# Kernel optimization log

Measured on AMD Instinct MI355X. Metric: run time of the kernel, lower is better.

The kernel has to match this reference:

```python
import jax, jax.numpy as jnp
import numpy as np

B, N_VIS, N_TOT, D, H, DEPTH = 4, 512, 2048, 768, 8, 2
HID = 3072  # int(D * 4.0)
TOKEN_DIM = 768


def setup_inputs() -> dict:
    key = jax.random.key(0)
    ks = jax.random.split(key, 20)
    s = 0.02
    # mask: exactly N_VIS True per row (visible positions), random placement
    u = jax.random.uniform(ks[0], (B, N_TOT))
    rank = jnp.argsort(jnp.argsort(u, axis=1), axis=1)
    mask = rank < N_VIS
    inp = {
        'visible_tokens': jax.random.normal(ks[1], (B, N_VIS, D), jnp.float32),
        'mask': mask,
        'mask_token': jax.random.normal(ks[2], (D,), jnp.float32) * s,
        'gamma1': jnp.ones((DEPTH, D), jnp.float32),
        'beta1': jnp.zeros((DEPTH, D), jnp.float32),
        'Wqkv': jax.random.normal(ks[3], (DEPTH, 3 * D, D), jnp.float32) * s,
        'bqkv': jnp.zeros((DEPTH, 3 * D), jnp.float32),
        'Wo': jax.random.normal(ks[4], (DEPTH, D, D), jnp.float32) * s,
        'bo': jnp.zeros((DEPTH, D), jnp.float32),
        'gamma2': jnp.ones((DEPTH, D), jnp.float32),
        'beta2': jnp.zeros((DEPTH, D), jnp.float32),
        'W1': jax.random.normal(ks[5], (DEPTH, HID, D), jnp.float32) * s,
        'b1': jnp.zeros((DEPTH, HID), jnp.float32),
        'W2': jax.random.normal(ks[6], (DEPTH, D, HID), jnp.float32) * s,
        'b2': jnp.zeros((DEPTH, D), jnp.float32),
        'gn': jnp.ones((D,), jnp.float32),
        'gb': jnp.zeros((D,), jnp.float32),
        'Wdec': jax.random.normal(ks[7], (TOKEN_DIM, D), jnp.float32) * s,
        'bdec': jnp.zeros((TOKEN_DIM,), jnp.float32),
    }
    return inp


def layer_norm(x, g, b, eps=1e-5):
    mu = jnp.mean(x, axis=-1, keepdims=True)
    var = jnp.var(x, axis=-1, keepdims=True)
    return (x - mu) * jax.lax.rsqrt(var + eps) * g + b


def mha(x, Wqkv, bqkv, Wo, bo):
    Bq, N, Dm = x.shape
    dh = Dm // H
    qkv = x @ Wqkv.T + bqkv  # (B,N,3D)
    q, k, v = jnp.split(qkv, 3, axis=-1)
    q = q.reshape(Bq, N, H, dh).transpose(0, 2, 1, 3)
    k = k.reshape(Bq, N, H, dh).transpose(0, 2, 1, 3)
    v = v.reshape(Bq, N, H, dh).transpose(0, 2, 1, 3)
    scores = jnp.einsum('bhqd,bhkd->bhqk', q, k) / jnp.sqrt(jnp.float32(dh))
    attn = jax.nn.softmax(scores, axis=-1)
    out = jnp.einsum('bhqk,bhkd->bhqd', attn, v)
    out = out.transpose(0, 2, 1, 3).reshape(Bq, N, Dm)
    return out @ Wo.T + bo


def decoder_block(x, g1, be1, Wqkv, bqkv, Wo, bo, g2, be2, W1f, b1f, W2f, b2f):
    x = x + mha(layer_norm(x, g1, be1), Wqkv, bqkv, Wo, bo)
    h = layer_norm(x, g2, be2)
    h = jax.nn.gelu(h @ W1f.T + b1f, approximate=False)
    return x + h @ W2f.T + b2f


def reference(visible_tokens, mask, mask_token, gamma1, beta1, Wqkv, bqkv, Wo, bo,
              gamma2, beta2, W1, b1, W2, b2, gn, gb, Wdec, bdec):
    # Vectorized in-order scatter: position n gets visible token #(count of True in mask[:, :n+1]) - 1
    idx = jnp.clip(jnp.cumsum(mask.astype(jnp.int32), axis=1) - 1, 0, N_VIS - 1)  # (B, N_TOT)
    gathered = jnp.take_along_axis(visible_tokens, idx[..., None], axis=1)  # (B, N_TOT, D)
    x = jnp.where(mask[..., None], gathered, mask_token)
    for i in range(DEPTH):
        x = decoder_block(x, gamma1[i], beta1[i], Wqkv[i], bqkv[i], Wo[i], bo[i],
                          gamma2[i], beta2[i], W1[i], b1[i], W2[i], b2[i])
    x = layer_norm(x, gn, gb)
    return x @ Wdec.T + bdec  # (B, N_TOT, token_dim)
```

## Files before the change

### kernel.cpp

```cpp
#include <hip/hip_runtime.h>
#include <stdint.h>

typedef __attribute__((ext_vector_type(8))) __bf16 bf16x8;
typedef __attribute__((ext_vector_type(4))) float f32x4;

#define DEVI static __device__ __forceinline__

#define QK_SCALE 0.10206207261596577f

DEVI uint16_t f2bf(float f){
  union{float f; uint32_t u;} v; v.f=f;
  uint32_t u = v.u;
  uint32_t r = u + 0x7FFFu + ((u>>16)&1u);
  return (uint16_t)(r>>16);
}
DEVI void gload16(const void* g, void* l){
  __builtin_amdgcn_global_load_lds((const __attribute__((address_space(1))) unsigned int*)g,
                                   (__attribute__((address_space(3))) unsigned int*)l, 16, 0, 0);
}


__global__ void cvt4_f32_bf16(const float* __restrict__ a, int na, uint16_t* __restrict__ oa,
                              const float* __restrict__ b, int nb, uint16_t* __restrict__ ob,
                              const float* __restrict__ c, int nc, uint16_t* __restrict__ oc,
                              const float* __restrict__ d, int nd, uint16_t* __restrict__ od){
  int total = na+nb+nc+nd;
  int stride = gridDim.x*blockDim.x;
  for(int i = blockIdx.x*blockDim.x + threadIdx.x; i<total; i+=stride){
    int j = i;
    if(j < na){ oa[j] = f2bf(a[j]); continue; }
    j -= na;
    if(j < nb){ ob[j] = f2bf(b[j]); continue; }
    j -= nb;
    if(j < nc){ oc[j] = f2bf(c[j]); continue; }
    j -= nc;
    od[j] = f2bf(d[j]);
  }
}

__global__ void cvt_wqkv(const float* __restrict__ in, uint16_t* __restrict__ out){
  const int n = 2*2304*768;
  int i = blockIdx.x*blockDim.x + threadIdx.x;
  int stride = gridDim.x*blockDim.x;
  for(; i<n; i+=stride){
    float v = in[i];
    if(((i/768) % 2304) < 768) v *= QK_SCALE;
    out[i] = f2bf(v);
  }
}

__global__ void scale_bqkv(const float* __restrict__ in, float* __restrict__ out){
  int i = blockIdx.x*blockDim.x + threadIdx.x;
  if(i < 2*2304){
    float v = in[i];
    if((i % 2304) < 768) v *= QK_SCALE;
    out[i] = v;
  }
}

__global__ void detect_mask(const uint8_t* __restrict__ mask, int* __restrict__ flag){
  __shared__ int cnt;
  if(threadIdx.x==0) cnt=0;
  __syncthreads();
  int c=0;
  for(int i=threadIdx.x;i<2048;i+=blockDim.x) c += (mask[i]!=0) ? 1 : 0;
  atomicAdd(&cnt, c);
  __syncthreads();
  if(threadIdx.x==0) *flag = (cnt==512) ? 1 : 0;
}

__global__ void scatter_idx(const void* __restrict__ maskp, const int* __restrict__ flag,
                            int* __restrict__ idx, uint8_t* __restrict__ mb){
  int b = blockIdx.x;
  int t = threadIdx.x;
  int f = *flag;
  const uint8_t* m8  = (const uint8_t*)maskp + (size_t)b*2048;
  const int*     m32 = (const int*)maskp + (size_t)b*2048;
  int v[8]; int s=0;
  for(int j=0;j<8;j++){ int n=t*8+j; int mv = f ? (m8[n]!=0) : (m32[n]!=0); v[j]=mv; s+=mv; }
  __shared__ int ps[256];
  ps[t]=s; __syncthreads();
  int acc=0;
  for(int i=0;i<t;i++) acc += ps[i];
  int cum=acc;
  for(int j=0;j<8;j++){
    int n=t*8+j;
    cum += v[j];
    int id = cum-1; id = id<0?0:(id>511?511:id);
    idx[(size_t)b*2048+n]=id;
    mb[(size_t)b*2048+n]=(uint8_t)v[j];
  }
}

__global__ void build_x(const float* __restrict__ vis, const float* __restrict__ mtok,
                        const int* __restrict__ idx, const uint8_t* __restrict__ mb,
                        float* __restrict__ x){
  int bn = blockIdx.x;
  int b = bn>>11;
  int id = idx[bn]; int m = mb[bn];
  const float* src = m ? (vis + ((size_t)b*512 + id)*768) : mtok;
  float* dst = x + (size_t)bn*768;
  for(int d=threadIdx.x; d<768; d+=256) dst[d] = src[d];
}

__global__ __launch_bounds__(256) void ln_kernel(const float* __restrict__ x,
                const float* __restrict__ g, const float* __restrict__ be,
                uint16_t* __restrict__ out){
  int row = blockIdx.x; int t = threadIdx.x;
  const float* xr = x + (size_t)row*768;
  float a0=xr[t], a1=xr[t+256], a2=xr[t+512];
  float s=a0+a1+a2, q=a0*a0+a1*a1+a2*a2;
  for(int off=32; off>0; off>>=1){ s+=__shfl_xor(s,off,64); q+=__shfl_xor(q,off,64); }
  __shared__ float sh[8];
  int w=t>>6, l=t&63;
  if(l==0){ sh[w]=s; sh[4+w]=q; }
  __syncthreads();
  s = sh[0]+sh[1]+sh[2]+sh[3];
  q = sh[4]+sh[5]+sh[6]+sh[7];
  float mean = s*(1.f/768.f);
  float var  = q*(1.f/768.f) - mean*mean;
  float rstd = rsqrtf(var + 1e-5f);
  uint16_t* orow = out + (size_t)row*768;
  orow[t]     = f2bf((a0-mean)*rstd*g[t]     + be[t]);
  orow[t+256] = f2bf((a1-mean)*rstd*g[t+256] + be[t+256]);
  orow[t+512] = f2bf((a2-mean)*rstd*g[t+512] + be[t+512]);
}

__global__ __launch_bounds__(128) void vtrans_kernel(const uint16_t* __restrict__ qkv,
                                                     uint16_t* __restrict__ vt){
  int nc = blockIdx.x, bh = blockIdx.y;
  int b = bh >> 3, h = bh & 7;
  int d = threadIdx.x;
  if(d >= 96) return;
  const uint16_t* src = qkv + ((size_t)(b*2048 + nc*8))*2304 + 1536 + h*96 + d;
  uint16_t vbuf[8];
  #pragma unroll
  for(int j=0;j<8;j++) vbuf[j] = src[(size_t)j*2304];
  *(uint4*)&vt[((size_t)bh*96 + d)*2048 + nc*8] = *(const uint4*)vbuf;
}

template<int BM, int BN, int WGM, int WGN, int GELU, int OUTF32>
__global__ __launch_bounds__(WGM*WGN*64) void gemm_kernel(const uint16_t* __restrict__ A,
        const uint16_t* __restrict__ W, const float* __restrict__ bias,
        const float* __restrict__ resid, void* __restrict__ outp,
        int M, int N, int K){
  constexpr int THREADS = WGM*WGN*64;
  constexpr int WTM = BM/WGM, WTN = BN/WGN;
  constexpr int MFM = WTM/16, MFN = WTN/16;
  constexpr int NCA = BM*4/THREADS;
  constexpr int NCB = BN*4/THREADS;
  __shared__ uint16_t sA[2][BM*32];
  __shared__ uint16_t sB[2][BN*32];
  int tid = threadIdx.x;
  int l = tid & 63, w = tid >> 6;
  int row0 = blockIdx.x*BM, col0 = blockIdx.y*BN;
  int wm = w / WGN, wn = w % WGN;
  f32x4 zero = {0.f,0.f,0.f,0.f};
  f32x4 acc[MFM][MFN];
  #pragma unroll
  for(int m=0;m<MFM;m++)
    #pragma unroll
    for(int n=0;n<MFN;n++) acc[m][n]=zero;
  int lr = l&15, lk = (l>>4)*8;
  int nkt = K >> 5;

  const uint16_t* gaP[NCA]; int ldsA[NCA];
  const uint16_t* gbP[NCB]; int ldsB[NCB];
  #pragma unroll
  for(int c=0;c<NCA;c++){
    int cb = c*THREADS + w*64;
    int ch = cb + l;
    gaP[c] = A + (size_t)(row0 + (ch>>2))*K + (ch&3)*8;
    ldsA[c] = cb*16;
  }
  #pragma unroll
  for(int c=0;c<NCB;c++){
    int cb = c*THREADS + w*64;
    int ch = cb + l;
    gbP[c] = W + (size_t)(col0 + (ch>>2))*K + (ch&3)*8;
    ldsB[c] = cb*16;
  }

  #pragma unroll
  for(int c=0;c<NCA;c++) gload16(gaP[c], (char*)sA[0] + ldsA[c]);
  #pragma unroll
  for(int c=0;c<NCB;c++) gload16(gbP[c], (char*)sB[0] + ldsB[c]);
  __syncthreads();

  int cur = 0;
  for(int kt=0; kt<nkt; kt++){
    if(kt+1 < nkt){
      int k0 = (kt+1)*32;
      #pragma unroll
      for(int c=0;c<NCA;c++) gload16(gaP[c] + k0, (char*)sA[cur^1] + ldsA[c]);
      #pragma unroll
      for(int c=0;c<NCB;c++) gload16(gbP[c] + k0, (char*)sB[cur^1] + ldsB[c]);
    }
    bf16x8 af[MFM], bfr[MFN];
    #pragma unroll
    for(int m=0;m<MFM;m++) af[m]  = *(const bf16x8*)(sA[cur] + (wm*WTM + m*16 + lr)*32 + lk);
    #pragma unroll
    for(int n=0;n<MFN;n++) bfr[n] = *(const bf16x8*)(sB[cur] + (wn*WTN + n*16 + lr)*32 + lk);
    __builtin_amdgcn_s_setprio(1);
    #pragma unroll
    for(int m=0;m<MFM;m++)
      #pragma unroll
      for(int n=0;n<MFN;n++)
        acc[m][n] = __builtin_amdgcn_mfma_f32_16x16x32_bf16(af[m], bfr[n], acc[m][n], 0,0,0);
    __builtin_amdgcn_s_setprio(0);
    __syncthreads();
    cur ^= 1;
  }
  #pragma unroll
  for(int m=0;m<MFM;m++){
    int r0 = row0 + wm*WTM + m*16 + (l>>4)*4;
    #pragma unroll
    for(int n=0;n<MFN;n++){
      int cc = col0 + wn*WTN + n*16 + lr;
      float bv = bias[cc];
      #pragma unroll
      for(int i=0;i<4;i++){
        int r = r0+i;
        float v = acc[m][n][i] + bv;
        if(GELU) v = 0.5f*v*(1.0f + erff(v*0.70710678118f));
        if(resid) v += resid[(size_t)r*N + cc];
        if(OUTF32) ((float*)outp)[(size_t)r*N + cc] = v;
        else ((uint16_t*)outp)[(size_t)r*N + cc] = f2bf(v);
      }
    }
  }
}

__global__ __launch_bounds__(512) void attn_kernel(const uint16_t* __restrict__ qkv,
                                                   const uint16_t* __restrict__ vt,
                                                   uint16_t* __restrict__ out){
  int qt = blockIdx.x, bh = blockIdx.y;
  int b = bh >> 3, h = bh & 7;
  int tid = threadIdx.x, l = tid&63, w = tid>>6;
  __shared__ union ShMem {
    uint16_t Qs[128*104];
    struct { uint16_t K[2][64*128]; uint16_t V[2][96*64]; uint16_t Ps[128*72]; } s;
  } sh;
  const size_t rs = 2304;
  const uint16_t* qbase = qkv + ((size_t)(b*2048 + qt*128))*rs + h*96;
  const uint16_t* kbase = qkv + ((size_t)(b*2048))*rs + 768 + h*96;
  const uint16_t* vbase = vt + (size_t)bh*96*2048;

  #pragma unroll
  for(int it=0; it<3; it++){
    int c = it*512 + tid;
    int r = c/12, col = (c%12)*8;
    *(uint4*)&sh.Qs[r*104 + col] = *(const uint4*)(qbase + (size_t)r*rs + col);
  }
  __syncthreads();
  int lr = l&15, lk = (l>>4)*8;
  bf16x8 qf[3];
  #pragma unroll
  for(int ks=0;ks<3;ks++) qf[ks] = *(const bf16x8*)(sh.Qs + (w*16+lr)*104 + ks*32 + lk);
  __syncthreads();

  int ck1 = w*64 + l, ck2 = 512 + w*64 + l;
  int kr1 = ck1>>4, ks1 = ck1&15, kj1 = ks1 ^ (kr1&15); if(kj1>=12) kj1=0;
  int kr2 = ck2>>4, ks2 = ck2&15, kj2 = ks2 ^ (kr2&15); if(kj2>=12) kj2=0;
  const uint16_t* kp1 = kbase + (size_t)kr1*rs + kj1*8;
  const uint16_t* kp2 = kbase + (size_t)kr2*rs + kj2*8;
  int kl1 = (w*64)*16, kl2 = (512 + w*64)*16;
  int cv1 = w*64 + l;
  int vd1 = cv1>>3, vs1 = cv1&7, vj1 = vs1 ^ (vd1&7);
  const uint16_t* vp1 = vbase + (size_t)vd1*2048 + vj1*8;
  int vl1 = (w*64)*16;
  int cv2 = 512 + ((w&3)*64) + l;
  int vd2 = cv2>>3, vs2 = cv2&7, vj2 = vs2 ^ (vd2&7);
  const uint16_t* vp2 = vbase + (size_t)vd2*2048 + vj2*8;
  int vl2 = (512 + (w&3)*64)*16;

  auto dmaKV = [&](int buf){
    char* kb0 = (char*)sh.s.K[buf];
    char* vb0 = (char*)sh.s.V[buf];
    gload16(kp1, kb0 + kl1);
    gload16(kp2, kb0 + kl2);
    gload16(vp1, vb0 + vl1);
    if(w < 4) gload16(vp2, vb0 + vl2);
    kp1 += (size_t)64*rs; kp2 += (size_t)64*rs; vp1 += 64; vp2 += 64;
  };

  float l_run[4];
  f32x4 zero = {0.f,0.f,0.f,0.f};
  f32x4 accO[6];
  #pragma unroll
  for(int i=0;i<4;i++) l_run[i]=0.f;
  #pragma unroll
  for(int d=0;d<6;d++) accO[d]=zero;

  dmaKV(0);
  int cur = 0;
  for(int kt=0; kt<32; kt++){
    if(kt > 0) __builtin_amdgcn_s_barrier();
    if(kt+1 < 32){
      dmaKV(cur^1);
      if(w < 4) asm volatile("s_waitcnt vmcnt(4)" ::: "memory");
      else      asm volatile("s_waitcnt vmcnt(3)" ::: "memory");
    } else {
      asm volatile("s_waitcnt vmcnt(0)" ::: "memory");
    }
    __builtin_amdgcn_s_barrier();
    __builtin_amdgcn_sched_barrier(0);

    const uint16_t* Kc = sh.s.K[cur];
    const uint16_t* Vc = sh.s.V[cur];
    f32x4 accS[4];
    #pragma unroll
    for(int nf=0;nf<4;nf++) accS[nf]=zero;
    __builtin_amdgcn_s_setprio(1);
    #pragma unroll
    for(int ks=0;ks<3;ks++){
      bf16x8 q = qf[ks];
      #pragma unroll
      for(int nf=0;nf<4;nf++){
        int slot = (ks*4 + (l>>4)) ^ lr;
        bf16x8 kf = *(const bf16x8*)(Kc + (nf*16+lr)*128 + slot*8);
        accS[nf] = __builtin_amdgcn_mfma_f32_16x16x32_bf16(q, kf, accS[nf], 0,0,0);
      }
    }
    __builtin_amdgcn_s_setprio(0);
    #pragma unroll
    for(int i=0;i<4;i++){
      float ps = 0.f;
      #pragma unroll
      for(int nf=0;nf<4;nf++){
        float p = __expf(accS[nf][i]);
        ps += p;
        union{float f; uint32_t u;} pv; pv.f = p;
        sh.s.Ps[(w*16 + (l>>4)*4 + i)*72 + nf*16 + lr] = (uint16_t)(pv.u >> 16);
      }
      #pragma unroll
      for(int off=1;off<16;off<<=1) ps += __shfl_xor(ps, off, 64);
      l_run[i] += ps;
    }
    __builtin_amdgcn_s_setprio(1);
    #pragma unroll
    for(int c2=0;c2<2;c2++){
      bf16x8 pf = *(const bf16x8*)(sh.s.Ps + (w*16+lr)*72 + c2*32 + lk);
      #pragma unroll
      for(int d=0;d<6;d++){
        int slot = (c2*4 + (l>>4)) ^ (lr&7);
        bf16x8 vf = *(const bf16x8*)(Vc + (d*16+lr)*64 + slot*8);
        accO[d] = __builtin_amdgcn_mfma_f32_16x16x32_bf16(pf, vf, accO[d], 0,0,0);
      }
    }
    __builtin_amdgcn_s_setprio(0);
    cur ^= 1;
  }
  float rl[4];
  #pragma unroll
  for(int i=0;i<4;i++) rl[i] = 1.0f / l_run[i];
  uint16_t* obase = out + ((size_t)(b*2048 + qt*128 + w*16))*768 + h*96;
  #pragma unroll
  for(int d=0;d<6;d++){
    #pragma unroll
    for(int i=0;i<4;i++){
      int r = (l>>4)*4 + i;
      obase[(size_t)r*768 + d*16 + lr] = f2bf(accO[d][i] * rl[i]);
    }
  }
}


extern "C" void kernel_launch(void* const* d_in, const int* in_sizes, int n_in,
                              void* d_out, int out_size, void* d_ws, size_t ws_size,
                              hipStream_t stream){
  const float* vis   = (const float*)d_in[0];
  const void*  mask  = d_in[1];
  const float* mtok  = (const float*)d_in[2];
  const float* gamma1= (const float*)d_in[3];
  const float* beta1 = (const float*)d_in[4];
  const float* Wqkv  = (const float*)d_in[5];
  const float* bqkv  = (const float*)d_in[6];
  const float* Wo    = (const float*)d_in[7];
  const float* bo    = (const float*)d_in[8];
  const float* gamma2= (const float*)d_in[9];
  const float* beta2 = (const float*)d_in[10];
  const float* W1    = (const float*)d_in[11];
  const float* b1    = (const float*)d_in[12];
  const float* W2    = (const float*)d_in[13];
  const float* b2    = (const float*)d_in[14];
  const float* gn    = (const float*)d_in[15];
  const float* gb    = (const float*)d_in[16];
  const float* Wdec  = (const float*)d_in[17];
  const float* bdec  = (const float*)d_in[18];

  char* ws = (char*)d_ws;
  size_t off = 0;
  auto alloc = [&](size_t bytes)->void*{
    void* p = ws + off; off = (off + bytes + 255) & ~(size_t)255; return p;
  };
  int*      flag = (int*)alloc(4);
  int*      idx  = (int*)alloc(8192*4);
  uint8_t*  mb   = (uint8_t*)alloc(8192);
  float*    sbq  = (float*)alloc(2*2304*4);
  float*    x    = (float*)alloc((size_t)8192*768*4);
  uint16_t* lnb  = (uint16_t*)alloc((size_t)8192*768*2);
  uint16_t* qkvb = (uint16_t*)alloc((size_t)8192*3072*2);
  uint16_t* wq   = (uint16_t*)alloc((size_t)2*2304*768*2);
  uint16_t* wo   = (uint16_t*)alloc((size_t)2*768*768*2);
  uint16_t* w1   = (uint16_t*)alloc((size_t)2*3072*768*2);
  uint16_t* w2   = (uint16_t*)alloc((size_t)2*768*3072*2);
  uint16_t* wd   = (uint16_t*)alloc((size_t)768*768*2);
  uint16_t* vtb  = qkvb + (size_t)8192*2304;

  cvt_wqkv<<<1024,256,0,stream>>>(Wqkv, wq);
  scale_bqkv<<<18,256,0,stream>>>(bqkv, sbq);
  cvt4_f32_bf16<<<1024,256,0,stream>>>(Wo, 2*768*768, wo,
                                       W1, 2*3072*768, w1,
                                       W2, 2*768*3072, w2,
                                       Wdec, 768*768, wd);

  detect_mask<<<1,256,0,stream>>>((const uint8_t*)mask, flag);
  scatter_idx<<<4,256,0,stream>>>(mask, flag, idx, mb);
  build_x<<<8192,256,0,stream>>>(vis, mtok, idx, mb, x);

  for(int i=0;i<2;i++){
    ln_kernel<<<8192,256,0,stream>>>(x, gamma1+i*768, beta1+i*768, lnb);
    gemm_kernel<128,128,2,2,0,0><<<dim3(64,18),256,0,stream>>>(lnb, wq+(size_t)i*2304*768, sbq+i*2304,
                                                   nullptr, qkvb, 8192, 2304, 768);
    vtrans_kernel<<<dim3(256,32),128,0,stream>>>(qkvb, vtb);
    attn_kernel<<<dim3(16,32),512,0,stream>>>(qkvb, vtb, lnb);
    gemm_kernel<128,64,2,2,0,1><<<dim3(64,12),256,0,stream>>>(lnb, wo+(size_t)i*768*768, bo+i*768,
                                                  x, x, 8192, 768, 768);
    ln_kernel<<<8192,256,0,stream>>>(x, gamma2+i*768, beta2+i*768, lnb);
    gemm_kernel<128,128,2,2,1,0><<<dim3(64,24),256,0,stream>>>(lnb, w1+(size_t)i*3072*768, b1+i*3072,
                                                   nullptr, qkvb, 8192, 3072, 768);
    gemm_kernel<128,64,2,2,0,1><<<dim3(64,12),256,0,stream>>>(qkvb, w2+(size_t)i*768*3072, b2+i*768,
                                                  x, x, 8192, 768, 3072);
  }
  ln_kernel<<<8192,256,0,stream>>>(x, gn, gb, lnb);
  gemm_kernel<128,64,2,2,0,1><<<dim3(64,12),256,0,stream>>>(lnb, wd, bdec, nullptr, d_out, 8192, 768, 768);
}
```

Baseline: 697.6 us.

## Triple-buffer GEMM LDS loads with vmcnt waits; defer attention row-sum reduction

The GEMM main loop moves from double to triple buffering. Global-to-LDS loads are issued two k-tiles ahead, and explicit s_waitcnt vmcnt counts plus raw barriers replace the per-iteration __syncthreads, so memory latency is hidden better. In the attention kernel, the cross-lane shuffle reduction of softmax row sums moves out of the key loop into the epilogue, since summing per-lane partials first gives the same total. The cost is 50% more shared memory in the GEMM, which may reduce occupancy, and a fragile hand-coded wait count that must match the PT values the templates instantiate.

```diff
diff --git a/kernel.cpp b/kernel.cpp
--- a/kernel.cpp
+++ b/kernel.cpp
@@ -17,6 +17,13 @@
 DEVI void gload16(const void* g, void* l){
   __builtin_amdgcn_global_load_lds((const __attribute__((address_space(1))) unsigned int*)g,
                                    (__attribute__((address_space(3))) unsigned int*)l, 16, 0, 0);
+}
+template<int N> DEVI void waitvm(){
+  if constexpr(N>=8)      asm volatile("s_waitcnt vmcnt(8)" ::: "memory");
+  else if constexpr(N==6) asm volatile("s_waitcnt vmcnt(6)" ::: "memory");
+  else if constexpr(N==4) asm volatile("s_waitcnt vmcnt(4)" ::: "memory");
+  else if constexpr(N==3) asm volatile("s_waitcnt vmcnt(3)" ::: "memory");
+  else                    asm volatile("s_waitcnt vmcnt(0)" ::: "memory");
 }
 
 
@@ -149,8 +156,9 @@
   constexpr int MFM = WTM/16, MFN = WTN/16;
   constexpr int NCA = BM*4/THREADS;
   constexpr int NCB = BN*4/THREADS;
-  __shared__ uint16_t sA[2][BM*32];
-  __shared__ uint16_t sB[2][BN*32];
+  constexpr int PT  = NCA + NCB;
+  __shared__ uint16_t sA[3][BM*32];
+  __shared__ uint16_t sB[3][BN*32];
   int tid = threadIdx.x;
   int l = tid & 63, w = tid >> 6;
   int row0 = blockIdx.x*BM, col0 = blockIdx.y*BN;
@@ -180,27 +188,37 @@
     gbP[c] = W + (size_t)(col0 + (ch>>2))*K + (ch&3)*8;
     ldsB[c] = cb*16;
   }
-
-  #pragma unroll
-  for(int c=0;c<NCA;c++) gload16(gaP[c], (char*)sA[0] + ldsA[c]);
-  #pragma unroll
-  for(int c=0;c<NCB;c++) gload16(gbP[c], (char*)sB[0] + ldsB[c]);
-  __syncthreads();
+  auto stage = [&](int ktile, int b){
+    int k0 = ktile*32;
+    #pragma unroll
+    for(int c=0;c<NCA;c++) gload16(gaP[c] + k0, (char*)sA[b] + ldsA[c]);
+    #pragma unroll
+    for(int c=0;c<NCB;c++) gload16(gbP[c] + k0, (char*)sB[b] + ldsB[c]);
+  };
+
+  stage(0, 0);
+  if(nkt > 1) stage(1, 1);
 
   int cur = 0;
   for(int kt=0; kt<nkt; kt++){
-    if(kt+1 < nkt){
-      int k0 = (kt+1)*32;
-      #pragma unroll
-      for(int c=0;c<NCA;c++) gload16(gaP[c] + k0, (char*)sA[cur^1] + ldsA[c]);
-      #pragma unroll
-      for(int c=0;c<NCB;c++) gload16(gbP[c] + k0, (char*)sB[cur^1] + ldsB[c]);
-    }
+    if(kt > 0) __builtin_amdgcn_s_barrier();
+    if(kt+2 < nkt){
+      int nb = cur+2; if(nb>=3) nb-=3;
+      stage(kt+2, nb);
+    }
+    if(kt+2 < nkt)      waitvm<2*PT>();
+    else if(kt+1 < nkt) waitvm<PT>();
+    else                waitvm<0>();
+    __builtin_amdgcn_s_barrier();
+    __builtin_amdgcn_sched_barrier(0);
+
+    const uint16_t* pA = sA[cur];
+    const uint16_t* pB = sB[cur];
     bf16x8 af[MFM], bfr[MFN];
     #pragma unroll
-    for(int m=0;m<MFM;m++) af[m]  = *(const bf16x8*)(sA[cur] + (wm*WTM + m*16 + lr)*32 + lk);
-    #pragma unroll
-    for(int n=0;n<MFN;n++) bfr[n] = *(const bf16x8*)(sB[cur] + (wn*WTN + n*16 + lr)*32 + lk);
+    for(int m=0;m<MFM;m++) af[m]  = *(const bf16x8*)(pA + (wm*WTM + m*16 + lr)*32 + lk);
+    #pragma unroll
+    for(int n=0;n<MFN;n++) bfr[n] = *(const bf16x8*)(pB + (wn*WTN + n*16 + lr)*32 + lk);
     __builtin_amdgcn_s_setprio(1);
     #pragma unroll
     for(int m=0;m<MFM;m++)
@@ -208,8 +226,7 @@
       for(int n=0;n<MFN;n++)
         acc[m][n] = __builtin_amdgcn_mfma_f32_16x16x32_bf16(af[m], bfr[n], acc[m][n], 0,0,0);
     __builtin_amdgcn_s_setprio(0);
-    __syncthreads();
-    cur ^= 1;
+    cur = (cur==2) ? 0 : cur+1;
   }
   #pragma unroll
   for(int m=0;m<MFM;m++){
@@ -333,8 +350,6 @@
         union{float f; uint32_t u;} pv; pv.f = p;
         sh.s.Ps[(w*16 + (l>>4)*4 + i)*72 + nf*16 + lr] = (uint16_t)(pv.u >> 16);
       }
-      #pragma unroll
-      for(int off=1;off<16;off<<=1) ps += __shfl_xor(ps, off, 64);
       l_run[i] += ps;
     }
     __builtin_amdgcn_s_setprio(1);
@@ -353,7 +368,12 @@
   }
   float rl[4];
   #pragma unroll
-  for(int i=0;i<4;i++) rl[i] = 1.0f / l_run[i];
+  for(int i=0;i<4;i++){
+    float s = l_run[i];
+    #pragma unroll
+    for(int off=1;off<16;off<<=1) s += __shfl_xor(s, off, 64);
+    rl[i] = 1.0f / s;
+  }
   uint16_t* obase = out + ((size_t)(b*2048 + qt*128 + w*16))*768 + h*96;
   #pragma unroll
   for(int d=0;d<6;d++){
```

Result: faster. 666.6 us (-4.4%).
